# Kernel optimization log

Measured on AMD Instinct MI355X. Metric: run time of the kernel, lower is better.

Reference implementation:

```python
import jax, jax.numpy as jnp
from jax import lax
import numpy as np

B = 64          # batch
HW = 28         # image height/width (hardcoded in module)
LATENT = 256    # latent_size
LABEL = 10      # label_size
FEAT = 64 * HW * HW  # 50176, encoder/decoder fc feature dim


def _conv(x, w, pad):
    # x: [N,C,H,W], w: [O,I,kH,kW]
    return lax.conv_general_dilated(
        x, w, (1, 1), ((pad, pad), (pad, pad)),
        dimension_numbers=('NCHW', 'OIHW', 'NCHW'))


def _conv_transpose(x, w, b, pad):
    # ConvTranspose2d(stride=1, padding=pad) == conv with flipped, transposed
    # kernel and padding k-1-pad. w: [I,O,kH,kW] (torch ConvTranspose layout).
    k = w.shape[2]
    wt = jnp.flip(w, (2, 3)).transpose(1, 0, 2, 3)  # [O,I,kH,kW]
    return _conv(x, wt, k - 1 - pad) + b[None, :, None, None]


def _encoder(images, c1w, c1b, c2w, c2b, fcw, fcb):
    x = jax.nn.relu(_conv(images, c1w, 2) + c1b[None, :, None, None])
    x = jax.nn.relu(_conv(x, c2w, 2) + c2b[None, :, None, None])
    x = x.reshape(x.shape[0], FEAT)
    return jnp.tanh(x @ fcw.T + fcb)


def _decoder(z, fcw, fcb, ct2w, ct2b, ct1w, ct1b):
    x = jnp.arctanh(z)
    x = (x @ fcw.T + fcb).reshape(-1, 64, HW, HW)
    x = jax.nn.relu(_conv_transpose(x, ct2w, ct2b, 2))
    return _conv_transpose(x, ct1w, ct1b, 2)


def _hopfield_weight(patterns):
    # TrainHopfield: Hebbian outer-product sum with mean subtraction,
    # zero diagonal, normalized by number of patterns. One GEMM.
    rho = jnp.mean(patterns)
    t = patterns - rho                      # [L, latent]
    w = t.T @ t                             # [latent, latent]
    w = w - jnp.diag(jnp.diag(w))
    return w / patterns.shape[0]


def _cluster(s0, w):
    # Batched version of: iterate s = sign(w @ s) up to LATENT steps,
    # stopping per-sample when energy -s@w@s stops changing.
    def energy(s):
        return -jnp.einsum('bi,ij,bj->b', s, w, s)

    def step(carry, _):
        s, prev_e, done = carry
        new_s = jnp.sign(s @ w.T)           # w symmetric; per-sample w@s
        e = energy(new_s)
        s_next = jnp.where(done[:, None], s, new_s)
        prev_e_next = jnp.where(done, prev_e, e)
        done_next = done | (e == prev_e)
        return (s_next, prev_e_next, done_next), None

    init = (s0, energy(s0), jnp.zeros(s0.shape[0], dtype=bool))
    (s, _, _), _ = lax.scan(step, init, None, length=LATENT)
    return s


def setup_inputs() -> dict:
    key = jax.random.key(0)
    ks = jax.random.split(key, 12)
    s = 0.05
    f32 = jnp.float32
    return {
        'images': jax.random.normal(ks[0], (B, 1, HW, HW), f32),
        'enc_c1_w': jax.random.normal(ks[1], (32, 1, 5, 5), f32) * s,
        'enc_c1_b': jnp.zeros((32,), f32),
        'enc_c2_w': jax.random.normal(ks[2], (64, 32, 5, 5), f32) * s,
        'enc_c2_b': jnp.zeros((64,), f32),
        'enc_fc_w': jax.random.normal(ks[3], (LATENT, FEAT), f32) * 0.005,
        'enc_fc_b': jnp.zeros((LATENT,), f32),
        'dec_fc_w': jax.random.normal(ks[4], (FEAT, LATENT), f32) * s,
        'dec_fc_b': jnp.zeros((FEAT,), f32),
        'dec_ct2_w': jax.random.normal(ks[5], (64, 32, 5, 5), f32) * s,
        'dec_ct2_b': jnp.zeros((32,), f32),
        'dec_ct1_w': jax.random.normal(ks[6], (32, 1, 5, 5), f32) * s,
        'dec_ct1_b': jnp.zeros((1,), f32),
        'sm_w': jax.random.normal(ks[7], (LABEL, LATENT), f32) * s,
        'sm_b': jnp.zeros((LABEL,), f32),
        'label_latent': jnp.tanh(jax.random.normal(ks[8], (LABEL, LATENT), f32)),
    }


def reference(images, enc_c1_w, enc_c1_b, enc_c2_w, enc_c2_b, enc_fc_w,
              enc_fc_b, dec_fc_w, dec_fc_b, dec_ct2_w, dec_ct2_b, dec_ct1_w,
              dec_ct1_b, sm_w, sm_b, label_latent):
    z = _encoder(images, enc_c1_w, enc_c1_b, enc_c2_w, enc_c2_b,
                 enc_fc_w, enc_fc_b)                       # [B, latent]
    w = _hopfield_weight(jnp.sign(label_latent))           # [latent, latent]
    s0 = lax.stop_gradient(jnp.sign(z))                    # detached copy
    clustered = _cluster(s0, w)                            # [B, latent]
    cluster_probs = jax.nn.softmax(clustered @ label_latent.T, axis=1)
    class_probs = jax.nn.softmax(z @ sm_w.T + sm_b, axis=1)
    recon = _decoder(z, dec_fc_w, dec_fc_b, dec_ct2_w, dec_ct2_b,
                     dec_ct1_w, dec_ct1_b)                 # [B,1,28,28]
    return (cluster_probs, class_probs, recon)
```

## Files before the change

kernel.cpp:

```cpp
#include <hip/hip_runtime.h>
#include <hip/hip_bf16.h>
#include <math.h>

#define BATCH 64
#define HW 28
#define PIX 784
#define LATENT 256
#define LABEL 10
#define FEAT 50176
#define KS 98
#define TSTR 36

typedef __attribute__((ext_vector_type(8))) short bf16x8;
typedef __attribute__((ext_vector_type(4))) float f32x4;

__device__ __forceinline__ float sgnf(float v) {
    return (v > 0.f) ? 1.f : ((v < 0.f) ? -1.f : 0.f);
}

__device__ __forceinline__ short f2bf(float f) {
    union { float f; unsigned u; } v; v.f = f;
    unsigned r = v.u + 0x7FFF + ((v.u >> 16) & 1);
    return (short)(r >> 16);
}
__device__ __forceinline__ float bf2f(short s) {
    union { unsigned u; float f; } v; v.u = ((unsigned)(unsigned short)s) << 16;
    return v.f;
}

__device__ __forceinline__ void split3(const float* __restrict__ p,
                                       bf16x8& h, bf16x8& m, bf16x8& l) {
    float4 a = *(const float4*)p;
    float4 b = *(const float4*)(p + 4);
    float v[8] = {a.x, a.y, a.z, a.w, b.x, b.y, b.z, b.w};
    #pragma unroll
    for (int j = 0; j < 8; ++j) {
        short s0 = f2bf(v[j]); float r = v[j] - bf2f(s0);
        short s1 = f2bf(r);    float r2 = r - bf2f(s1);
        h[j] = s0; m[j] = s1; l[j] = f2bf(r2);
    }
}

template<int G, int FLIP>
__global__ __launch_bounds__(256) void conv5_k(const float* __restrict__ in,
                        const float* __restrict__ w,
                        const float* __restrict__ bias, float* __restrict__ out,
                        int IC, int OC, int relu) {
    int b = blockIdx.x, oc0 = blockIdx.y * G;
    __shared__ float plp[2][32 * TSTR];
    int tid = threadIdx.x;

    for (int t = tid; t < 2 * 32 * TSTR; t += 256) ((float*)plp)[t] = 0.f;

    bool actS = tid < 196;
    int ys = tid / 7, qs = tid % 7;

    int q = tid & 7, yy = tid >> 3;
    bool actC = (q < 7) && (yy < 28);
    int x0 = q * 4;

    float acc[G][4];
    #pragma unroll
    for (int g = 0; g < G; ++g)
        #pragma unroll
        for (int xi = 0; xi < 4; ++xi) acc[g][xi] = 0.f;

    __syncthreads();
    if (actS) {
        float4 v = *(const float4*)&in[((size_t)(b * IC + 0)) * PIX + tid * 4];
        *(float2*)&plp[0][(ys + 2) * TSTR + 4 * qs + 2] = make_float2(v.x, v.y);
        *(float2*)&plp[0][(ys + 2) * TSTR + 4 * qs + 4] = make_float2(v.z, v.w);
    }
    __syncthreads();

    for (int ic = 0; ic < IC; ++ic) {
        float4 vn;
        bool more = (ic + 1) < IC;
        if (more && actS)
            vn = *(const float4*)&in[((size_t)(b * IC + ic + 1)) * PIX + tid * 4];

        const float* tile = plp[ic & 1];
        if (actC) {
            #pragma unroll
            for (int dy = 0; dy < 5; ++dy) {
                float4 ra = *(const float4*)&tile[(yy + dy) * TSTR + x0];
                float4 rb = *(const float4*)&tile[(yy + dy) * TSTR + x0 + 4];
                float rw[8] = {ra.x, ra.y, ra.z, ra.w, rb.x, rb.y, rb.z, rb.w};
                #pragma unroll
                for (int g = 0; g < G; ++g) {
                    #pragma unroll
                    for (int dx = 0; dx < 5; ++dx) {
                        float wv = FLIP
                            ? w[((size_t)ic * OC + (oc0 + g)) * 25 + (4 - dy) * 5 + (4 - dx)]
                            : w[((size_t)(oc0 + g) * IC + ic) * 25 + dy * 5 + dx];
                        #pragma unroll
                        for (int xi = 0; xi < 4; ++xi)
                            acc[g][xi] += rw[xi + dx] * wv;
                    }
                }
            }
        }
        if (more && actS) {
            float* nt = plp[(ic + 1) & 1];
            *(float2*)&nt[(ys + 2) * TSTR + 4 * qs + 2] = make_float2(vn.x, vn.y);
            *(float2*)&nt[(ys + 2) * TSTR + 4 * qs + 4] = make_float2(vn.z, vn.w);
        }
        __syncthreads();
    }

    if (actC) {
        #pragma unroll
        for (int g = 0; g < G; ++g) {
            float bv = bias[oc0 + g];
            float4 o;
            o.x = acc[g][0] + bv;
            o.y = acc[g][1] + bv;
            o.z = acc[g][2] + bv;
            o.w = acc[g][3] + bv;
            if (relu) {
                o.x = fmaxf(o.x, 0.f); o.y = fmaxf(o.y, 0.f);
                o.z = fmaxf(o.z, 0.f); o.w = fmaxf(o.w, 0.f);
            }
            *(float4*)&out[((size_t)(b * OC + (oc0 + g))) * PIX + yy * HW + x0] = o;
        }
    }
}

__global__ __launch_bounds__(64) void c2_mfma_k(const short* __restrict__ xh,
                        const short* __restrict__ xm, const short* __restrict__ xl,
                        const short* __restrict__ wb,
                        const float* __restrict__ bias, float* __restrict__ out) {
    int b = blockIdx.x;
    int t0 = blockIdx.y * 4;
    int lane = threadIdx.x;
    int prow = lane & 15, kgrp = lane >> 4;

    f32x4 acc[4][4];
    #pragma unroll
    for (int pt = 0; pt < 4; ++pt)
        #pragma unroll
        for (int nt = 0; nt < 4; ++nt) acc[pt][nt] = (f32x4){0.f, 0.f, 0.f, 0.f};

    int py[4], px[4];
    bool ptv[4];
    #pragma unroll
    for (int pt = 0; pt < 4; ++pt) {
        int p = (t0 + pt) * 16 + prow;
        ptv[pt] = (t0 + pt) < 49;
        py[pt] = p / 28; px[pt] = p % 28;
    }

    for (int tap = 0; tap < 25; ++tap) {
        int dy = tap / 5 - 2, dx = tap % 5 - 2;
        const short* wt = wb + (size_t)tap * 2048;
        bf16x8 B0[4], B1[4], B2[4];
        #pragma unroll
        for (int nt = 0; nt < 4; ++nt) {
            int off = (nt * 16 + prow) * 32 + kgrp * 8;
            B0[nt] = *(const bf16x8*)&wt[off];
            B1[nt] = *(const bf16x8*)&wt[51200 + off];
            B2[nt] = *(const bf16x8*)&wt[102400 + off];
        }
        #pragma unroll
        for (int pt = 0; pt < 4; ++pt) {
            int ysrc = py[pt] + dy, xsrc = px[pt] + dx;
            bool valid = ptv[pt] && (ysrc >= 0) && (ysrc < 28) && (xsrc >= 0) && (xsrc < 28);
            bf16x8 ah = {0,0,0,0,0,0,0,0}, am = {0,0,0,0,0,0,0,0}, al = {0,0,0,0,0,0,0,0};
            if (valid) {
                size_t o = ((size_t)b * PIX + ysrc * 28 + xsrc) * 32 + kgrp * 8;
                ah = *(const bf16x8*)&xh[o];
                am = *(const bf16x8*)&xm[o];
                al = *(const bf16x8*)&xl[o];
            }
            #pragma unroll
            for (int nt = 0; nt < 4; ++nt) {
                acc[pt][nt] = __builtin_amdgcn_mfma_f32_16x16x32_bf16(ah, B0[nt], acc[pt][nt], 0, 0, 0);
                acc[pt][nt] = __builtin_amdgcn_mfma_f32_16x16x32_bf16(ah, B1[nt], acc[pt][nt], 0, 0, 0);
                acc[pt][nt] = __builtin_amdgcn_mfma_f32_16x16x32_bf16(am, B0[nt], acc[pt][nt], 0, 0, 0);
                acc[pt][nt] = __builtin_amdgcn_mfma_f32_16x16x32_bf16(ah, B2[nt], acc[pt][nt], 0, 0, 0);
                acc[pt][nt] = __builtin_amdgcn_mfma_f32_16x16x32_bf16(am, B1[nt], acc[pt][nt], 0, 0, 0);
                acc[pt][nt] = __builtin_amdgcn_mfma_f32_16x16x32_bf16(al, B0[nt], acc[pt][nt], 0, 0, 0);
            }
        }
    }

    __shared__ float ot[64][17];
    float bv = bias[lane];
    for (int pt = 0; pt < 4; ++pt) {
        if (!ptv[pt]) continue;
        #pragma unroll
        for (int nt = 0; nt < 4; ++nt)
            #pragma unroll
            for (int r = 0; r < 4; ++r)
                ot[nt * 16 + prow][kgrp * 4 + r] = acc[pt][nt][r];
        float* op = &out[((size_t)(b * 64 + lane)) * PIX + (t0 + pt) * 16];
        #pragma unroll
        for (int i = 0; i < 4; ++i) {
            float4 o;
            o.x = fmaxf(ot[lane][i * 4 + 0] + bv, 0.f);
            o.y = fmaxf(ot[lane][i * 4 + 1] + bv, 0.f);
            o.z = fmaxf(ot[lane][i * 4 + 2] + bv, 0.f);
            o.w = fmaxf(ot[lane][i * 4 + 3] + bv, 0.f);
            *(float4*)&op[i * 4] = o;
        }
    }
}

__global__ void xsplit3_k(const float* __restrict__ x, short* __restrict__ xh,
                          short* __restrict__ xm, short* __restrict__ xl) {
    __shared__ float lds[32][17];
    int b = blockIdx.x, pbase = blockIdx.y * 16;
    int t = threadIdx.x;
    if (t < 128) {
        int ic = t >> 2, pj = (t & 3) * 4;
        float4 v = *(const float4*)&x[((size_t)(b * 32 + ic)) * PIX + pbase + pj];
        lds[ic][pj + 0] = v.x; lds[ic][pj + 1] = v.y;
        lds[ic][pj + 2] = v.z; lds[ic][pj + 3] = v.w;
    }
    __syncthreads();
    int p = t >> 4, ic2 = (t & 15) * 2;
    size_t o = ((size_t)b * PIX + pbase + p) * 32 + ic2;
    short2 h, m, l;
    {
        float v = lds[ic2][p];
        short s0 = f2bf(v); float r = v - bf2f(s0);
        short s1 = f2bf(r); float r2 = r - bf2f(s1);
        h.x = s0; m.x = s1; l.x = f2bf(r2);
    }
    {
        float v = lds[ic2 + 1][p];
        short s0 = f2bf(v); float r = v - bf2f(s0);
        short s1 = f2bf(r); float r2 = r - bf2f(s1);
        h.y = s0; m.y = s1; l.y = f2bf(r2);
    }
    *(short2*)&xh[o] = h;
    *(short2*)&xm[o] = m;
    *(short2*)&xl[o] = l;
}

__global__ void wprep3_k(const float* __restrict__ w, short* __restrict__ wb) {
    int j = blockIdx.x * 256 + threadIdx.x;
    if (j < 51200) {
        int ic = j & 31;
        int oc = (j >> 5) & 63;
        int tap = j >> 11;
        float v = w[((size_t)oc * 32 + ic) * 25 + tap];
        short s0 = f2bf(v); float r = v - bf2f(s0);
        short s1 = f2bf(r); float r2 = r - bf2f(s1);
        wb[j] = s0;
        wb[51200 + j] = s1;
        wb[102400 + j] = f2bf(r2);
    }
}

__global__ __launch_bounds__(64) void ct2_mfma_k(const short* __restrict__ xb,
                        const short* __restrict__ wb,
                        const float* __restrict__ bias, float* __restrict__ out) {
    int b = blockIdx.x;
    int pbase = blockIdx.y * 16;
    int lane = threadIdx.x;
    int prow = lane & 15;
    int kgrp = lane >> 4;
    int p = pbase + prow;
    int py = p / 28, px = p % 28;

    f32x4 acc0 = {0.f, 0.f, 0.f, 0.f};
    f32x4 acc1 = {0.f, 0.f, 0.f, 0.f};

    for (int tap = 0; tap < 25; ++tap) {
        int dy = tap / 5 - 2, dx = tap % 5 - 2;
        int ysrc = py + dy, xsrc = px + dx;
        bool valid = (ysrc >= 0) && (ysrc < 28) && (xsrc >= 0) && (xsrc < 28);
        int ps = ysrc * 28 + xsrc;

        bf16x8 a0 = {0,0,0,0,0,0,0,0}, a1 = {0,0,0,0,0,0,0,0};
        if (valid) {
            const bf16x8* ap = (const bf16x8*)&xb[((size_t)b * PIX + ps) * 64 + kgrp * 8];
            a0 = ap[0];
            a1 = ap[4];
        }
        const short* wt = &wb[(size_t)tap * 32 * 64];
        int oc_l = lane & 15;
        bf16x8 b00 = *(const bf16x8*)&wt[oc_l * 64 + kgrp * 8];
        bf16x8 b01 = *(const bf16x8*)&wt[oc_l * 64 + 32 + kgrp * 8];
        bf16x8 b10 = *(const bf16x8*)&wt[(16 + oc_l) * 64 + kgrp * 8];
        bf16x8 b11 = *(const bf16x8*)&wt[(16 + oc_l) * 64 + 32 + kgrp * 8];

        acc0 = __builtin_amdgcn_mfma_f32_16x16x32_bf16(a0, b00, acc0, 0, 0, 0);
        acc0 = __builtin_amdgcn_mfma_f32_16x16x32_bf16(a1, b01, acc0, 0, 0, 0);
        acc1 = __builtin_amdgcn_mfma_f32_16x16x32_bf16(a0, b10, acc1, 0, 0, 0);
        acc1 = __builtin_amdgcn_mfma_f32_16x16x32_bf16(a1, b11, acc1, 0, 0, 0);
    }

    __shared__ float ot[32][16];
    int drow = (lane >> 4) * 4;
    #pragma unroll
    for (int r = 0; r < 4; ++r) {
        ot[lane & 15][drow + r]        = acc0[r];
        ot[16 + (lane & 15)][drow + r] = acc1[r];
    }
    __syncthreads();
    int oc = lane >> 1, ph = (lane & 1) * 8;
    float bv = bias[oc];
    float4 o0, o1;
    o0.x = fmaxf(ot[oc][ph + 0] + bv, 0.f);
    o0.y = fmaxf(ot[oc][ph + 1] + bv, 0.f);
    o0.z = fmaxf(ot[oc][ph + 2] + bv, 0.f);
    o0.w = fmaxf(ot[oc][ph + 3] + bv, 0.f);
    o1.x = fmaxf(ot[oc][ph + 4] + bv, 0.f);
    o1.y = fmaxf(ot[oc][ph + 5] + bv, 0.f);
    o1.z = fmaxf(ot[oc][ph + 6] + bv, 0.f);
    o1.w = fmaxf(ot[oc][ph + 7] + bv, 0.f);
    float* op = &out[((size_t)(b * 32 + oc)) * PIX + pbase + ph];
    *(float4*)&op[0] = o0;
    *(float4*)&op[4] = o1;
}

__global__ void wprep_k(const float* __restrict__ w, short* __restrict__ wb) {
    int j = blockIdx.x * 256 + threadIdx.x;
    if (j < 25 * 32 * 64) {
        int ic = j & 63;
        int oc = (j >> 6) & 31;
        int tap = j >> 11;
        int dyi = tap / 5, dxi = tap % 5;
        wb[j] = f2bf(w[((size_t)ic * 32 + oc) * 25 + (4 - dyi) * 5 + (4 - dxi)]);
    }
}

__global__ void xpose16_k(const short* __restrict__ y16, short* __restrict__ xb) {
    __shared__ short lds[64][16];
    int b = blockIdx.x, pbase = blockIdx.y * 16;
    int t = threadIdx.x;
    {
        int ic = t >> 2, pj = (t & 3) * 4;
        short4 v = *(const short4*)&y16[((size_t)(b * 64 + ic)) * PIX + pbase + pj];
        lds[ic][pj + 0] = v.x;
        lds[ic][pj + 1] = v.y;
        lds[ic][pj + 2] = v.z;
        lds[ic][pj + 3] = v.w;
    }
    __syncthreads();
    {
        int p = t >> 4, icq = (t & 15) * 4;
        short4 s;
        s.x = lds[icq + 0][p];
        s.y = lds[icq + 1][p];
        s.z = lds[icq + 2][p];
        s.w = lds[icq + 3][p];
        *(short4*)&xb[((size_t)b * PIX + pbase + p) * 64 + icq] = s;
    }
}

__global__ __launch_bounds__(512) void enc_fc_mfma_k(const float* __restrict__ x,
                        const float* __restrict__ w, float* __restrict__ part) {
    int ks = blockIdx.x;
    int kbase = ks * 512;
    int tid = threadIdx.x;
    int lane = tid & 63, wv = tid >> 6;
    int prow = lane & 15, kgrp = lane >> 4;

    f32x4 acc[4][2];
    #pragma unroll
    for (int mt = 0; mt < 4; ++mt)
        #pragma unroll
        for (int ntl = 0; ntl < 2; ++ntl) acc[mt][ntl] = (f32x4){0.f, 0.f, 0.f, 0.f};

    for (int kt = 0; kt < 16; ++kt) {
        int kof = kbase + kt * 32 + kgrp * 8;
        bf16x8 ah[4], am[4], al[4];
        #pragma unroll
        for (int mt = 0; mt < 4; ++mt)
            split3(&x[(size_t)(mt * 16 + prow) * FEAT + kof], ah[mt], am[mt], al[mt]);
        #pragma unroll
        for (int ntl = 0; ntl < 2; ++ntl) {
            bf16x8 bh, bm, bl;
            split3(&w[(size_t)(wv * 32 + ntl * 16 + prow) * FEAT + kof], bh, bm, bl);
            #pragma unroll
            for (int mt = 0; mt < 4; ++mt) {
                acc[mt][ntl] = __builtin_amdgcn_mfma_f32_16x16x32_bf16(ah[mt], bh, acc[mt][ntl], 0, 0, 0);
                acc[mt][ntl] = __builtin_amdgcn_mfma_f32_16x16x32_bf16(ah[mt], bm, acc[mt][ntl], 0, 0, 0);
                acc[mt][ntl] = __builtin_amdgcn_mfma_f32_16x16x32_bf16(am[mt], bh, acc[mt][ntl], 0, 0, 0);
                acc[mt][ntl] = __builtin_amdgcn_mfma_f32_16x16x32_bf16(ah[mt], bl, acc[mt][ntl], 0, 0, 0);
                acc[mt][ntl] = __builtin_amdgcn_mfma_f32_16x16x32_bf16(am[mt], bm, acc[mt][ntl], 0, 0, 0);
                acc[mt][ntl] = __builtin_amdgcn_mfma_f32_16x16x32_bf16(al[mt], bh, acc[mt][ntl], 0, 0, 0);
            }
        }
    }

    __shared__ float ot[64 * 257];
    #pragma unroll
    for (int mt = 0; mt < 4; ++mt)
        #pragma unroll
        for (int ntl = 0; ntl < 2; ++ntl)
            #pragma unroll
            for (int r = 0; r < 4; ++r) {
                int m = mt * 16 + kgrp * 4 + r;
                int n = wv * 32 + ntl * 16 + prow;
                ot[m * 257 + n] = acc[mt][ntl][r];
            }
    __syncthreads();
    int m = tid >> 3, c0 = (tid & 7) * 4;
    float* pp = &part[(size_t)ks * BATCH * LATENT + m * 256];
    #pragma unroll
    for (int i = 0; i < 8; ++i) {
        int n = c0 + i * 32;
        *(float4*)&pp[n] = *(float4*)&ot[m * 257 + n];
    }
}

__global__ void enc_fc_fin_k(const float* __restrict__ part, const float* __restrict__ bias,
                             float* __restrict__ z, short* __restrict__ xah,
                             short* __restrict__ xam) {
    int m = blockIdx.x;
    int n = threadIdx.x;
    int idx = m * 256 + n;
    float a = bias[n];
    for (int ksi = 0; ksi < KS; ++ksi) a += part[(size_t)ksi * BATCH * LATENT + idx];
    float zv = tanhf(a);
    z[idx] = zv;
    float xv = atanhf(zv);
    short h = f2bf(xv);
    xah[idx] = h;
    xam[idx] = f2bf(xv - bf2f(h));
}

__global__ void hop_rho_k(const float* __restrict__ ll, float* __restrict__ rho_out) {
    float p = 0.f;
    for (int t = threadIdx.x; t < LABEL * LATENT; t += 256) p += sgnf(ll[t]);
    __shared__ float red[8];
    for (int o = 32; o; o >>= 1) p += __shfl_down(p, o, 64);
    if ((threadIdx.x & 63) == 0) red[threadIdx.x >> 6] = p;
    __syncthreads();
    if (threadIdx.x == 0)
        rho_out[0] = (red[0] + red[1] + red[2] + red[3]) / (float)(LABEL * LATENT);
}

__global__ void hop_w_k(const float* __restrict__ ll, const float* __restrict__ rho_p,
                        float* __restrict__ wout) {
    int i = blockIdx.x, j = threadIdx.x;
    float rho = rho_p[0];
    float acc = 0.f;
    #pragma unroll
    for (int l = 0; l < LABEL; ++l) {
        float a = sgnf(ll[l * LATENT + i]) - rho;
        float b = sgnf(ll[l * LATENT + j]) - rho;
        acc += a * b;
    }
    wout[i * LATENT + j] = (i == j) ? 0.f : acc / 10.f;
}

__global__ __launch_bounds__(1024) void cluster_k(const float* __restrict__ z,
                          const float* __restrict__ w,
                          const float* __restrict__ ll, float* __restrict__ out) {
    int b = blockIdx.x;
    int t = threadIdx.x;
    int i = t & 255;
    int q = t >> 8;
    int lane = t & 63;
    int wvid = t >> 6;

    __shared__ float s_sh[LATENT];
    __shared__ float part[1024];
    __shared__ float red[4];
    __shared__ float cflag[4];
    __shared__ int ctl_sh;
    __shared__ float logit[LABEL];

    float wreg[64];
    #pragma unroll
    for (int jj = 0; jj < 64; ++jj)
        wreg[jj] = w[(q * 64 + jj) * LATENT + i];

    float s_cur = 0.f, s_old = 2.f, v = 0.f;
    float e_prev = 0.f;
    if (q == 0) {
        s_cur = sgnf(z[b * LATENT + i]);
        s_sh[i] = s_cur;
    }
    __syncthreads();

    {
        float p0 = 0.f, p1 = 0.f;
        #pragma unroll
        for (int jj = 0; jj < 64; jj += 2) {
            p0 += wreg[jj]     * s_sh[q * 64 + jj];
            p1 += wreg[jj + 1] * s_sh[q * 64 + jj + 1];
        }
        part[t] = p0 + p1;
    }
    __syncthreads();
    if (q == 0) {
        v = part[i] + part[i + 256] + part[i + 512] + part[i + 768];
        float p = s_cur * v;
        #pragma unroll
        for (int o = 32; o; o >>= 1) p += __shfl_down(p, o, 64);
        if (lane == 0) red[wvid] = p;
    }
    __syncthreads();
    if (t == 0) e_prev = -(red[0] + red[1] + red[2] + red[3]);

    for (int it = 0; it < LATENT; ++it) {
        if (q == 0) {
            float ns = sgnf(v);
            unsigned long long m = __ballot(ns == s_old);
            if (lane == 0) cflag[wvid] = (m == ~0ull) ? 1.f : 0.f;
            s_sh[i] = ns;
            s_old = s_cur;
            s_cur = ns;
        }
        __syncthreads();
        {
            float p0 = 0.f, p1 = 0.f;
            #pragma unroll
            for (int jj = 0; jj < 64; jj += 2) {
                p0 += wreg[jj]     * s_sh[q * 64 + jj];
                p1 += wreg[jj + 1] * s_sh[q * 64 + jj + 1];
            }
            part[t] = p0 + p1;
        }
        __syncthreads();
        if (q == 0) {
            v = part[i] + part[i + 256] + part[i + 512] + part[i + 768];
            float p = s_cur * v;
            #pragma unroll
            for (int o = 32; o; o >>= 1) p += __shfl_down(p, o, 64);
            if (lane == 0) red[wvid] = p;
        }
        __syncthreads();
        if (t == 0) {
            float e = -(red[0] + red[1] + red[2] + red[3]);
            int c = 0;
            if (e == e_prev) c = 1;
            else if (it >= 1 && cflag[0] != 0.f && cflag[1] != 0.f &&
                     cflag[2] != 0.f && cflag[3] != 0.f)
                c = (((LATENT - 1 - it) & 1) == 0) ? 2 : 3;
            else e_prev = e;
            ctl_sh = c;
        }
        __syncthreads();
        int c = ctl_sh;
        if (c != 0) {
            if (c == 3 && q == 0) s_sh[i] = s_old;
            break;
        }
    }
    __syncthreads();

    if (wvid < LABEL) {
        float p = 0.f;
        #pragma unroll
        for (int r = 0; r < 4; ++r)
            p += s_sh[r * 64 + lane] * ll[wvid * LATENT + r * 64 + lane];
        #pragma unroll
        for (int o = 32; o; o >>= 1) p += __shfl_down(p, o, 64);
        if (lane == 0) logit[wvid] = p;
    }
    __syncthreads();
    if (t == 0) {
        float mx = logit[0];
        for (int c = 1; c < LABEL; ++c) mx = fmaxf(mx, logit[c]);
        float ex[LABEL];
        float s = 0.f;
        for (int c = 0; c < LABEL; ++c) { ex[c] = expf(logit[c] - mx); s += ex[c]; }
        for (int c = 0; c < LABEL; ++c) out[b * LABEL + c] = ex[c] / s;
    }
}

__device__ __forceinline__ float block_sum256(float p, float* red) {
    __syncthreads();
    for (int o = 32; o; o >>= 1) p += __shfl_down(p, o, 64);
    if ((threadIdx.x & 63) == 0) red[threadIdx.x >> 6] = p;
    __syncthreads();
    return red[0] + red[1] + red[2] + red[3];
}

__global__ void class_k(const float* __restrict__ z, const float* __restrict__ smw,
                        const float* __restrict__ smb, float* __restrict__ out) {
    int b = blockIdx.x;
    int i = threadIdx.x;
    __shared__ float red[8];
    __shared__ float logit[LABEL];
    float zi = z[b * LATENT + i];
    for (int c = 0; c < LABEL; ++c) {
        float p = zi * smw[c * LATENT + i];
        float t = block_sum256(p, red);
        if (i == 0) logit[c] = t + smb[c];
    }
    __syncthreads();
    if (i == 0) {
        float mx = logit[0];
        for (int c = 1; c < LABEL; ++c) mx = fmaxf(mx, logit[c]);
        float ex[LABEL];
        float s = 0.f;
        for (int c = 0; c < LABEL; ++c) { ex[c] = expf(logit[c] - mx); s += ex[c]; }
        for (int c = 0; c < LABEL; ++c) out[b * LABEL + c] = ex[c] / s;
    }
}

__global__ __launch_bounds__(256) void dec_fc_mfma_k(const short* __restrict__ xah,
                         const short* __restrict__ xam,
                         const float* __restrict__ w,
                         const float* __restrict__ bias, short* __restrict__ y16) {
    int tid = threadIdx.x;
    int lane = tid & 63, wv = tid >> 6;
    int prow = lane & 15, kgrp = lane >> 4;
    int n0 = blockIdx.x * 64;
    int nb = n0 + wv * 16;

    f32x4 acc[4];
    #pragma unroll
    for (int mi = 0; mi < 4; ++mi) acc[mi] = (f32x4){0.f, 0.f, 0.f, 0.f};

    for (int kc = 0; kc < 8; ++kc) {
        int kof = kc * 32 + kgrp * 8;
        const float* wp = &w[(size_t)(nb + prow) * LATENT + kof];
        float4 w0 = *(const float4*)&wp[0];
        float4 w1 = *(const float4*)&wp[4];
        bf16x8 bf;
        bf[0] = f2bf(w0.x); bf[1] = f2bf(w0.y); bf[2] = f2bf(w0.z); bf[3] = f2bf(w0.w);
        bf[4] = f2bf(w1.x); bf[5] = f2bf(w1.y); bf[6] = f2bf(w1.z); bf[7] = f2bf(w1.w);
        #pragma unroll
        for (int mi = 0; mi < 4; ++mi) {
            bf16x8 ah = *(const bf16x8*)&xah[(mi * 16 + prow) * LATENT + kof];
            bf16x8 am = *(const bf16x8*)&xam[(mi * 16 + prow) * LATENT + kof];
            acc[mi] = __builtin_amdgcn_mfma_f32_16x16x32_bf16(ah, bf, acc[mi], 0, 0, 0);
            acc[mi] = __builtin_amdgcn_mfma_f32_16x16x32_bf16(am, bf, acc[mi], 0, 0, 0);
        }
    }

    __shared__ short ot[64 * 72];
    float bv = bias[nb + prow];
    #pragma unroll
    for (int mi = 0; mi < 4; ++mi)
        #pragma unroll
        for (int r = 0; r < 4; ++r) {
            int m = mi * 16 + kgrp * 4 + r;
            ot[m * 72 + wv * 16 + prow] = f2bf(acc[mi][r] + bv);
        }
    __syncthreads();
    int m = tid >> 2, q = tid & 3;
    #pragma unroll
    for (int i = 0; i < 2; ++i) {
        *(int4*)&y16[(size_t)m * FEAT + n0 + i * 32 + q * 8] =
            *(int4*)&ot[m * 72 + i * 32 + q * 8];
    }
}

extern "C" void kernel_launch(void* const* d_in, const int* in_sizes, int n_in,
                              void* d_out, int out_size, void* d_ws, size_t ws_size,
                              hipStream_t stream) {
    const float* images   = (const float*)d_in[0];
    const float* c1w      = (const float*)d_in[1];
    const float* c1b      = (const float*)d_in[2];
    const float* c2w      = (const float*)d_in[3];
    const float* c2b      = (const float*)d_in[4];
    const float* efw      = (const float*)d_in[5];
    const float* efb      = (const float*)d_in[6];
    const float* dfw      = (const float*)d_in[7];
    const float* dfb      = (const float*)d_in[8];
    const float* ct2w     = (const float*)d_in[9];
    const float* ct2b     = (const float*)d_in[10];
    const float* ct1w     = (const float*)d_in[11];
    const float* ct1b     = (const float*)d_in[12];
    const float* smw      = (const float*)d_in[13];
    const float* smb      = (const float*)d_in[14];
    const float* ll       = (const float*)d_in[15];

    float* out = (float*)d_out;
    float* ws  = (float*)d_ws;

    float* big0 = ws;
    float* big1 = ws + 3211264;
    float* z    = ws + 3211264 + 1605632 + 458752;
    float* whop = z + BATCH * LATENT;
    float* rho  = whop + LATENT * LATENT;
    float* xsa  = rho + 4;
    short* xah  = (short*)xsa;
    short* xam  = xah + 16384;
    short* xbf  = (short*)(xsa + 16384);
    short* wbf  = (short*)(xsa + 16384 + 1605632);
    short* xh3  = xbf;
    short* xm3  = xbf + 1605632;
    short* xl3  = (short*)(xsa + 16384 + 1605632 + 25600);
    short* wb3  = xl3 + 1605632;
    short* y16  = (short*)big0;
    float* part = (float*)xbf;

    conv5_k<4,0><<<dim3(BATCH, 8), 256, 0, stream>>>(images, c1w, c1b, big1, 1, 32, 1);
    wprep3_k<<<200, 256, 0, stream>>>(c2w, wb3);
    xsplit3_k<<<dim3(BATCH, 49), 256, 0, stream>>>(big1, xh3, xm3, xl3);
    c2_mfma_k<<<dim3(BATCH, 13), 64, 0, stream>>>(xh3, xm3, xl3, wb3, c2b, big0);
    enc_fc_mfma_k<<<KS, 512, 0, stream>>>(big0, efw, part);
    enc_fc_fin_k<<<BATCH, 256, 0, stream>>>(part, efb, z, xah, xam);

    hop_rho_k<<<1, 256, 0, stream>>>(ll, rho);
    hop_w_k<<<LATENT, 256, 0, stream>>>(ll, rho, whop);
    cluster_k<<<BATCH, 1024, 0, stream>>>(z, whop, ll, out);
    class_k<<<BATCH, 256, 0, stream>>>(z, smw, smb, out + 640);

    wprep_k<<<200, 256, 0, stream>>>(ct2w, wbf);
    dec_fc_mfma_k<<<FEAT / 64, 256, 0, stream>>>(xah, xam, dfw, dfb, y16);
    xpose16_k<<<dim3(BATCH, 49), 256, 0, stream>>>(y16, xbf);
    ct2_mfma_k<<<dim3(BATCH, 49), 64, 0, stream>>>(xbf, wbf, ct2b, big1);
    conv5_k<1,1><<<dim3(BATCH, 1), 256, 0, stream>>>(big1, ct1w, ct1b, out + 1280, 32, 1, 0);
}
```

Baseline: 296.5 us.

## Split conv2 taps across four waves and encoder FC over output halves

The conv2 MFMA kernel now runs four waves per block, each handling a strided subset of the 25 kernel taps. Partial accumulators are reduced through shared memory before the bias/ReLU epilogue. The encoder FC kernel gets a second grid dimension that splits the 256 outputs into two halves, so each wave owns one 16-column tile, doubling block count. This raises parallelism and occupancy on the GPU, at the cost of an LDS reduction in conv2 and reloading the activation tiles twice in the FC kernel.

New measurement: 305.4 us. 1.03x slower.

```diff
diff --git a/kernel.cpp b/kernel.cpp
--- a/kernel.cpp
+++ b/kernel.cpp
@@ -126,13 +126,15 @@
     }
 }
 
-__global__ __launch_bounds__(64) void c2_mfma_k(const short* __restrict__ xh,
+__global__ __launch_bounds__(256) void c2_mfma_k(const short* __restrict__ xh,
                         const short* __restrict__ xm, const short* __restrict__ xl,
                         const short* __restrict__ wb,
                         const float* __restrict__ bias, float* __restrict__ out) {
     int b = blockIdx.x;
     int t0 = blockIdx.y * 4;
-    int lane = threadIdx.x;
+    int tid = threadIdx.x;
+    int wv = tid >> 6;
+    int lane = tid & 63;
     int prow = lane & 15, kgrp = lane >> 4;
 
     f32x4 acc[4][4];
@@ -150,7 +152,7 @@
         py[pt] = p / 28; px[pt] = p % 28;
     }
 
-    for (int tap = 0; tap < 25; ++tap) {
+    for (int tap = wv; tap < 25; tap += 4) {
         int dy = tap / 5 - 2, dx = tap % 5 - 2;
         const short* wt = wb + (size_t)tap * 2048;
         bf16x8 B0[4], B1[4], B2[4];
@@ -184,24 +186,51 @@
         }
     }
 
-    __shared__ float ot[64][17];
-    float bv = bias[lane];
-    for (int pt = 0; pt < 4; ++pt) {
-        if (!ptv[pt]) continue;
-        #pragma unroll
-        for (int nt = 0; nt < 4; ++nt)
+    __shared__ float red[3][64][64];
+    if (wv > 0) {
+        #pragma unroll
+        for (int pt = 0; pt < 4; ++pt)
             #pragma unroll
-            for (int r = 0; r < 4; ++r)
-                ot[nt * 16 + prow][kgrp * 4 + r] = acc[pt][nt][r];
-        float* op = &out[((size_t)(b * 64 + lane)) * PIX + (t0 + pt) * 16];
-        #pragma unroll
-        for (int i = 0; i < 4; ++i) {
-            float4 o;
-            o.x = fmaxf(ot[lane][i * 4 + 0] + bv, 0.f);
-            o.y = fmaxf(ot[lane][i * 4 + 1] + bv, 0.f);
-            o.z = fmaxf(ot[lane][i * 4 + 2] + bv, 0.f);
-            o.w = fmaxf(ot[lane][i * 4 + 3] + bv, 0.f);
-            *(float4*)&op[i * 4] = o;
+            for (int nt = 0; nt < 4; ++nt)
+                #pragma unroll
+                for (int r = 0; r < 4; ++r)
+                    red[wv - 1][lane][pt * 16 + nt * 4 + r] = acc[pt][nt][r];
+    }
+    __syncthreads();
+    if (wv == 0) {
+        #pragma unroll
+        for (int pt = 0; pt < 4; ++pt)
+            #pragma unroll
+            for (int nt = 0; nt < 4; ++nt)
+                #pragma unroll
+                for (int r = 0; r < 4; ++r) {
+                    int ix = pt * 16 + nt * 4 + r;
+                    float s = acc[pt][nt][r];
+                    s += red[0][lane][ix];
+                    s += red[1][lane][ix];
+                    s += red[2][lane][ix];
+                    acc[pt][nt][r] = s;
+                }
+
+        __shared__ float ot[64][17];
+        float bv = bias[lane];
+        for (int pt = 0; pt < 4; ++pt) {
+            if (!ptv[pt]) continue;
+            #pragma unroll
+            for (int nt = 0; nt < 4; ++nt)
+                #pragma unroll
+                for (int r = 0; r < 4; ++r)
+                    ot[nt * 16 + prow][kgrp * 4 + r] = acc[pt][nt][r];
+            float* op = &out[((size_t)(b * 64 + lane)) * PIX + (t0 + pt) * 16];
+            #pragma unroll
+            for (int i = 0; i < 4; ++i) {
+                float4 o;
+                o.x = fmaxf(ot[lane][i * 4 + 0] + bv, 0.f);
+                o.y = fmaxf(ot[lane][i * 4 + 1] + bv, 0.f);
+                o.z = fmaxf(ot[lane][i * 4 + 2] + bv, 0.f);
+                o.w = fmaxf(ot[lane][i * 4 + 3] + bv, 0.f);
+                *(float4*)&op[i * 4] = o;
+            }
         }
     }
 }
@@ -354,57 +383,49 @@
 __global__ __launch_bounds__(512) void enc_fc_mfma_k(const float* __restrict__ x,
                         const float* __restrict__ w, float* __restrict__ part) {
     int ks = blockIdx.x;
+    int nh = blockIdx.y;
     int kbase = ks * 512;
     int tid = threadIdx.x;
     int lane = tid & 63, wv = tid >> 6;
     int prow = lane & 15, kgrp = lane >> 4;
-
-    f32x4 acc[4][2];
-    #pragma unroll
-    for (int mt = 0; mt < 4; ++mt)
-        #pragma unroll
-        for (int ntl = 0; ntl < 2; ++ntl) acc[mt][ntl] = (f32x4){0.f, 0.f, 0.f, 0.f};
+    int nrow = nh * 128 + wv * 16 + prow;
+
+    f32x4 acc[4];
+    #pragma unroll
+    for (int mt = 0; mt < 4; ++mt) acc[mt] = (f32x4){0.f, 0.f, 0.f, 0.f};
 
     for (int kt = 0; kt < 16; ++kt) {
         int kof = kbase + kt * 32 + kgrp * 8;
-        bf16x8 ah[4], am[4], al[4];
-        #pragma unroll
-        for (int mt = 0; mt < 4; ++mt)
-            split3(&x[(size_t)(mt * 16 + prow) * FEAT + kof], ah[mt], am[mt], al[mt]);
-        #pragma unroll
-        for (int ntl = 0; ntl < 2; ++ntl) {
-            bf16x8 bh, bm, bl;
-            split3(&w[(size_t)(wv * 32 + ntl * 16 + prow) * FEAT + kof], bh, bm, bl);
-            #pragma unroll
-            for (int mt = 0; mt < 4; ++mt) {
-                acc[mt][ntl] = __builtin_amdgcn_mfma_f32_16x16x32_bf16(ah[mt], bh, acc[mt][ntl], 0, 0, 0);
-                acc[mt][ntl] = __builtin_amdgcn_mfma_f32_16x16x32_bf16(ah[mt], bm, acc[mt][ntl], 0, 0, 0);
-                acc[mt][ntl] = __builtin_amdgcn_mfma_f32_16x16x32_bf16(am[mt], bh, acc[mt][ntl], 0, 0, 0);
-                acc[mt][ntl] = __builtin_amdgcn_mfma_f32_16x16x32_bf16(ah[mt], bl, acc[mt][ntl], 0, 0, 0);
-                acc[mt][ntl] = __builtin_amdgcn_mfma_f32_16x16x32_bf16(am[mt], bm, acc[mt][ntl], 0, 0, 0);
-                acc[mt][ntl] = __builtin_amdgcn_mfma_f32_16x16x32_bf16(al[mt], bh, acc[mt][ntl], 0, 0, 0);
-            }
-        }
-    }
-
-    __shared__ float ot[64 * 257];
+        bf16x8 bh, bm, bl;
+        split3(&w[(size_t)nrow * FEAT + kof], bh, bm, bl);
+        #pragma unroll
+        for (int mt = 0; mt < 4; ++mt) {
+            bf16x8 ah, am, al;
+            split3(&x[(size_t)(mt * 16 + prow) * FEAT + kof], ah, am, al);
+            acc[mt] = __builtin_amdgcn_mfma_f32_16x16x32_bf16(ah, bh, acc[mt], 0, 0, 0);
+            acc[mt] = __builtin_amdgcn_mfma_f32_16x16x32_bf16(ah, bm, acc[mt], 0, 0, 0);
+            acc[mt] = __builtin_amdgcn_mfma_f32_16x16x32_bf16(am, bh, acc[mt], 0, 0, 0);
+            acc[mt] = __builtin_amdgcn_mfma_f32_16x16x32_bf16(ah, bl, acc[mt], 0, 0, 0);
+            acc[mt] = __builtin_amdgcn_mfma_f32_16x16x32_bf16(am, bm, acc[mt], 0, 0, 0);
+            acc[mt] = __builtin_amdgcn_mfma_f32_16x16x32_bf16(al, bh, acc[mt], 0, 0, 0);
+        }
+    }
+
+    __shared__ float ot[64 * 129];
     #pragma unroll
     for (int mt = 0; mt < 4; ++mt)
         #pragma unroll
-        for (int ntl = 0; ntl < 2; ++ntl)
-            #pragma unroll
-            for (int r = 0; r < 4; ++r) {
-                int m = mt * 16 + kgrp * 4 + r;
-                int n = wv * 32 + ntl * 16 + prow;
-                ot[m * 257 + n] = acc[mt][ntl][r];
-            }
+        for (int r = 0; r < 4; ++r) {
+            int m = mt * 16 + kgrp * 4 + r;
+            ot[m * 129 + wv * 16 + prow] = acc[mt][r];
+        }
     __syncthreads();
     int m = tid >> 3, c0 = (tid & 7) * 4;
-    float* pp = &part[(size_t)ks * BATCH * LATENT + m * 256];
-    #pragma unroll
-    for (int i = 0; i < 8; ++i) {
+    float* pp = &part[(size_t)ks * BATCH * LATENT + m * 256 + nh * 128];
+    #pragma unroll
+    for (int i = 0; i < 4; ++i) {
         int n = c0 + i * 32;
-        *(float4*)&pp[n] = *(float4*)&ot[m * 257 + n];
+        *(float4*)&pp[n] = *(float4*)&ot[m * 129 + n];
     }
 }
 
@@ -689,8 +710,8 @@
     conv5_k<4,0><<<dim3(BATCH, 8), 256, 0, stream>>>(images, c1w, c1b, big1, 1, 32, 1);
     wprep3_k<<<200, 256, 0, stream>>>(c2w, wb3);
     xsplit3_k<<<dim3(BATCH, 49), 256, 0, stream>>>(big1, xh3, xm3, xl3);
-    c2_mfma_k<<<dim3(BATCH, 13), 64, 0, stream>>>(xh3, xm3, xl3, wb3, c2b, big0);
-    enc_fc_mfma_k<<<KS, 512, 0, stream>>>(big0, efw, part);
+    c2_mfma_k<<<dim3(BATCH, 13), 256, 0, stream>>>(xh3, xm3, xl3, wb3, c2b, big0);
+    enc_fc_mfma_k<<<dim3(KS, 2), 512, 0, stream>>>(big0, efw, part);
     enc_fc_fin_k<<<BATCH, 256, 0, stream>>>(part, efb, z, xah, xam);
 
     hop_rho_k<<<1, 256, 0, stream>>>(ll, rho);
```
